# Performance work log

Hardware: AMD Instinct MI355X
Metric: run time of the kernel (lower is better)

## Reference

```python
import jax, jax.numpy as jnp
import numpy as np

APP = 21  # app_num, hard-coded in the original forward (x[..., -21:])


def setup_inputs() -> dict:
    key = jax.random.key(0)
    S, F = 1024, 64            # seq_len, feature_num
    INP = F - 21 + 1           # input_size = 44
    H, E = 1024, 512           # hidden_size, embedding_size
    OUT = 1
    ks = jax.random.split(key, 16)
    s = 0.02
    return {
        "x": jax.random.normal(ks[0], (1, S, F), jnp.float32),
        "W_ie": jax.random.normal(ks[1], (E, INP), jnp.float32) * s,
        "b_ie": jnp.zeros((E,), jnp.float32),
        "W_te": jax.random.normal(ks[2], (E, APP * H), jnp.float32) * s,
        "b_te": jnp.zeros((E,), jnp.float32),
        "W_ih0": jax.random.normal(ks[3], (4 * H, 2 * E), jnp.float32) * s,
        "W_hh0": jax.random.normal(ks[4], (4 * H, H), jnp.float32) * s,
        "b_ih0": jnp.zeros((4 * H,), jnp.float32),
        "b_hh0": jnp.zeros((4 * H,), jnp.float32),
        "W_ih1": jax.random.normal(ks[5], (4 * H, H), jnp.float32) * s,
        "W_hh1": jax.random.normal(ks[6], (4 * H, H), jnp.float32) * s,
        "b_ih1": jnp.zeros((4 * H,), jnp.float32),
        "b_hh1": jnp.zeros((4 * H,), jnp.float32),
        "W_out": jax.random.normal(ks[7], (OUT, APP * H), jnp.float32) * s,
        "b_out": jnp.zeros((OUT,), jnp.float32),
    }


def _lstm_cell(xt, h, c, W_ih, W_hh, b_ih, b_hh):
    # PyTorch gate order: i, f, g, o
    gates = xt @ W_ih.T + b_ih + h @ W_hh.T + b_hh  # [APP, 4H]
    i, f, g, o = jnp.split(gates, 4, axis=-1)
    c_new = jax.nn.sigmoid(f) * c + jax.nn.sigmoid(i) * jnp.tanh(g)
    h_new = jax.nn.sigmoid(o) * jnp.tanh(c_new)
    return h_new, c_new


def reference(x, W_ie, b_ie, W_te, b_te, W_ih0, W_hh0, b_ih0, b_hh0,
              W_ih1, W_hh1, b_ih1, b_hh1, W_out, b_out):
    # eval-mode: dropout is identity (both embedding dropout and LSTM inter-layer dropout)
    S = x.shape[1]
    H = W_hh0.shape[1]
    E = W_ie.shape[0]

    feats = x[0, :, :-APP]                                   # [S, F-21]
    feats = jnp.broadcast_to(feats[:, None, :], (S, APP, feats.shape[-1]))
    app = x[0, :, -APP:][:, :, None]                          # [S, 21, 1]
    input_data = jnp.concatenate([feats, app], axis=-1)       # [S, 21, INP]

    h0 = jnp.zeros((APP, H), x.dtype)
    c0 = jnp.zeros((APP, H), x.dtype)
    h1 = jnp.zeros((APP, H), x.dtype)
    c1 = jnp.zeros((APP, H), x.dtype)

    def step(carry, xt):
        h0, c0, h1, c1 = carry
        # social tensor: last-layer hidden flattened, identical row for all 21 apps
        social = h1.reshape(-1)                               # [21*H]
        te = jax.nn.relu(W_te @ social + b_te)                # [E]
        ie = jax.nn.relu(xt @ W_ie.T + b_ie)                  # [21, E]
        z = jnp.concatenate([ie, jnp.broadcast_to(te, (APP, E))], axis=-1)  # [21, 2E]
        h0n, c0n = _lstm_cell(z, h0, c0, W_ih0, W_hh0, b_ih0, b_hh0)
        h1n, c1n = _lstm_cell(h0n, h1, c1, W_ih1, W_hh1, b_ih1, b_hh1)
        out = W_out @ h1n.reshape(-1) + b_out                 # [output_size]
        return (h0n, c0n, h1n, c1n), out

    (h0, c0, h1, c1), outs = jax.lax.scan(step, (h0, c0, h1, c1), input_data)
    outputs = outs[None, :, :]                                # [1, S, output_size]
    hidden = jnp.stack([h0, h1], axis=0)                      # [num_layer, 21, H]
    cell = jnp.stack([c0, c1], axis=0)
    return outputs, (hidden, cell)
```

## Files before the change

kernel.cpp:

```cpp
#include <hip/hip_runtime.h>
#include <math.h>


#define NBLK 256
#define NTHR 512
#define HTHR 256
#define SEQ  1024
#define HID  1024
#define EMB  512
#define NAG  21
#define NH   21504

#define IE_OFF  0
#define H0_OFF  11010048
#define H1_OFF  (H0_OFF + 2*NH)
#define TE_OFF  (H1_OFF + 2*NH)
#define BAR_OFF (TE_OFF + 512)
#define ZTOT    (4*NH + 512 + 1024)

#define HROW   1152
#define IEROW  576
#define OFF_H    0
#define OFF_IE   24192
#define OFF_TE   36288
#define OFF_PART 36864
#define OFF_B0   39888
#define OFF_B1   39904
#define OFF_RED  39920
#define OFF_ABT  39936
#define LDS_F    39952

#define REP4(M)  M(0) M(1) M(2) M(3)
#define REP8(M)  REP4(M) M(4) M(5) M(6) M(7)
#define REP10(M) REP8(M) M(8) M(9)
#define REP16(M) REP8(M) M(8) M(9) M(10) M(11) M(12) M(13) M(14) M(15)
#define REP40(M) REP16(M) M(16) M(17) M(18) M(19) M(20) M(21) M(22) M(23) \
  M(24) M(25) M(26) M(27) M(28) M(29) M(30) M(31) M(32) M(33) M(34) M(35) \
  M(36) M(37) M(38) M(39)

typedef unsigned u32x4 __attribute__((ext_vector_type(4)));
typedef unsigned u32x2 __attribute__((ext_vector_type(2)));

struct Params {
  const float *x, *W_ie, *b_ie, *W_te, *b_te;
  const float *W_ih0, *W_hh0, *b_ih0, *b_hh0;
  const float *W_ih1, *W_hh1, *b_ih1, *b_hh1;
  const float *W_out, *b_out;
  float *out, *ws;
};

__device__ __forceinline__ float sigf(float v) { return 1.0f / (1.0f + expf(-v)); }

__device__ __forceinline__ float ald(const float* p) {
  return __hip_atomic_load(p, __ATOMIC_RELAXED, __HIP_MEMORY_SCOPE_AGENT);
}
__device__ __forceinline__ void ast(float* p, float v) {
  __hip_atomic_store(p, v, __ATOMIC_RELAXED, __HIP_MEMORY_SCOPE_AGENT);
}
__device__ __forceinline__ unsigned f2bf(float f) {
  unsigned u = __float_as_uint(f);
  return (u + 0x7fffu + ((u >> 16) & 1u)) >> 16;
}

__device__ __forceinline__ float block_sum(float v, float* red) {
  #pragma unroll
  for (int off = 32; off > 0; off >>= 1) v += __shfl_down(v, off, 64);
  const int w = threadIdx.x >> 6;
  if ((threadIdx.x & 63) == 0) red[w] = v;
  __syncthreads();
  float r = 0.f;
  #pragma unroll
  for (int i = 0; i < NTHR / 64; ++i) r += red[i];
  __syncthreads();
  return r;
}

__device__ __forceinline__ void block_sum2(float& v0, float& v1, float* red) {
  #pragma unroll
  for (int off = 32; off > 0; off >>= 1) {
    v0 += __shfl_down(v0, off, 64);
    v1 += __shfl_down(v1, off, 64);
  }
  const int w = threadIdx.x >> 6;
  if ((threadIdx.x & 63) == 0) { red[2 * w] = v0; red[2 * w + 1] = v1; }
  __syncthreads();
  v0 = ((red[0] + red[2]) + (red[4] + red[6])) + ((red[8] + red[10]) + (red[12] + red[14]));
  v1 = ((red[1] + red[3]) + (red[5] + red[7])) + ((red[9] + red[11]) + (red[13] + red[15]));
  __syncthreads();
}

__device__ __forceinline__ bool grid_barrier(unsigned* bars, unsigned ep, int b,
                                             float* ldsf) {
  __syncthreads();
  if (threadIdx.x == 0) {
    float abortv = 0.f;
    unsigned* grel = bars + 512 + ((unsigned)b >> 4) * 32;
    if (__hip_atomic_load(bars + 300, __ATOMIC_RELAXED, __HIP_MEMORY_SCOPE_AGENT) != 0u) {
      abortv = 1.f;
    } else {
      asm volatile("s_waitcnt vmcnt(0)" ::: "memory");
      unsigned* gc = bars + 16 + ((unsigned)b >> 4) * 16;
      unsigned old = __hip_atomic_fetch_add(gc, 1u, __ATOMIC_RELAXED, __HIP_MEMORY_SCOPE_AGENT);
      if (old == ep * 16u - 1u) {
        unsigned rold = __hip_atomic_fetch_add(bars + 16 + 256, 1u, __ATOMIC_RELAXED, __HIP_MEMORY_SCOPE_AGENT);
        if (rold == ep * 16u - 1u) {
          #pragma unroll
          for (int g = 0; g < 16; ++g)
            __hip_atomic_store(bars + 512 + g * 32, ep, __ATOMIC_RELAXED, __HIP_MEMORY_SCOPE_AGENT);
        }
      }
      unsigned spins = 0u;
      while (__hip_atomic_load(grel, __ATOMIC_RELAXED, __HIP_MEMORY_SCOPE_AGENT) < ep) {
        __builtin_amdgcn_s_sleep(8);
        if (++spins > 1000000u) {
          __hip_atomic_store(bars + 300, 1u, __ATOMIC_RELAXED, __HIP_MEMORY_SCOPE_AGENT);
          abortv = 1.f;
          break;
        }
        if ((spins & 255u) == 0u &&
            __hip_atomic_load(bars + 300, __ATOMIC_RELAXED, __HIP_MEMORY_SCOPE_AGENT) != 0u) {
          abortv = 1.f;
          break;
        }
      }
      asm volatile("" ::: "memory");
    }
    ldsf[OFF_ABT] = abortv;
  }
  __syncthreads();
  return ldsf[OFF_ABT] != 0.f;
}

__global__ void sl_init(float* ws) {
  int tid = blockIdx.x * blockDim.x + threadIdx.x;
  int stride = gridDim.x * blockDim.x;
  for (int i = tid; i < ZTOT; i += stride) ws[H0_OFF + i] = 0.0f;
}

__global__ void sl_ie(const float* __restrict__ x, const float* __restrict__ W_ie,
                      const float* __restrict__ b_ie, float* __restrict__ ws) {
  const int t = blockIdx.x;
  const int tid = threadIdx.x;
  __shared__ float xs[64];
  __shared__ float base[EMB];
  __shared__ float w43[EMB];
  if (tid < 64) xs[tid] = x[t * 64 + tid];
  __syncthreads();
  for (int e = tid; e < EMB; e += HTHR) {
    const float* wr = W_ie + e * 44;
    float acc = b_ie[e];
    #pragma unroll
    for (int k = 0; k < 43; ++k) acc += xs[k] * wr[k];
    base[e] = acc;
    w43[e] = wr[43];
  }
  __syncthreads();
  float* iep = ws + IE_OFF + (size_t)t * (NAG * EMB);
  for (int idx = tid; idx < NAG * EMB; idx += HTHR) {
    int a = idx >> 9, e = idx & 511;
    float v = base[e] + xs[43 + a] * w43[e];
    iep[idx] = v > 0.0f ? v : 0.0f;
  }
}

#define SLDQ(q) { const float4* ap = hs4 + 10 * tid + (q); \
  asm volatile("global_load_dwordx4 %0, %1, off sc0" : "=v"(sv[q]) : "v"(ap)); }
#define SSTQ(q) { int i0 = 40 * tid + 4 * (q); int aa = i0 >> 10; int cc = i0 & 1023; \
  float2 f0v; f0v.x = __uint_as_float(sv[q][0]); f0v.y = __uint_as_float(sv[q][1]); \
  *(float2*)&lds[OFF_H + aa * HROW + 36 * (cc >> 5) + (cc & 31)] = f0v; \
  int i1 = i0 + 2; int a1i = i1 >> 10; int c1i = i1 & 1023; \
  float2 f1v; f1v.x = __uint_as_float(sv[q][2]); f1v.y = __uint_as_float(sv[q][3]); \
  *(float2*)&lds[OFF_H + a1i * HROW + 36 * (c1i >> 5) + (c1i & 31)] = f1v; }
#define STAGE_H(SRC) { \
  const float4* hs4 = (const float4*)(SRC); \
  u32x4 sv[10]; u32x2 sv2; \
  REP10(SLDQ) \
  { const float* ap = (const float*)(SRC) + 20480 + 2 * tid; \
    asm volatile("global_load_dwordx2 %0, %1, off sc0" : "=v"(sv2) : "v"(ap)); } \
  asm volatile("s_waitcnt vmcnt(0)" ::: "memory"); \
  __builtin_amdgcn_sched_barrier(0); \
  REP10(SSTQ) \
  { int i2 = 20480 + 2 * tid; int aa = i2 >> 10; int cc = i2 & 1023; float2 ff; \
    ff.x = __uint_as_float(sv2[0]); ff.y = __uint_as_float(sv2[1]); \
    *(float2*)&lds[OFF_H + aa * HROW + 36 * (cc >> 5) + (cc & 31)] = ff; } }

__global__ void __launch_bounds__(NTHR)
__attribute__((amdgpu_waves_per_eu(2, 2)))
sl_main(Params P) {
  const int b = blockIdx.x;
  const int tid = threadIdx.x;
  float* ws = P.ws;
  float* wste = ws + TE_OFF;
  unsigned* bars = (unsigned*)(ws + BAR_OFF);

  __shared__ float lds[LDS_F];

  const int lane = tid & 63;
  const int wav  = tid >> 6;
  const int n    = tid & 15;
  const int ks   = tid >> 4;
  const int grow = (n >> 2) * HID + 4 * b + (n & 3);

  float w0[64];
  {
    const float* s0 = (ks < 16) ? (P.W_ih0 + (size_t)grow * 1024 + 64 * ks)
                                : (P.W_hh0 + (size_t)grow * 1024 + 64 * (ks - 16));
#define LW0(i) { float4 v = *(const float4*)(s0 + 4*(i)); \
    w0[4*(i)] = v.x; w0[4*(i)+1] = v.y; w0[4*(i)+2] = v.z; w0[4*(i)+3] = v.w; }
    REP16(LW0)
  }
  float w1a[32], w1b[32];
  {
    const float* s1 = P.W_ih1 + (size_t)grow * 1024 + 32 * ks;
    const float* s2 = P.W_hh1 + (size_t)grow * 1024 + 32 * ks;
#define LW1(i) { float4 v = *(const float4*)(s1 + 4*(i)); \
    w1a[4*(i)] = v.x; w1a[4*(i)+1] = v.y; w1a[4*(i)+2] = v.z; w1a[4*(i)+3] = v.w; \
    float4 u = *(const float4*)(s2 + 4*(i)); \
    w1b[4*(i)] = u.x; w1b[4*(i)+1] = u.y; w1b[4*(i)+2] = u.z; w1b[4*(i)+3] = u.w; }
    REP8(LW1)
  }
  unsigned wtepk[42];
  {
    const float* wt0 = P.W_te + (size_t)(2 * b) * NH;
#define LWT(k) { float f0 = wt0[40*tid + (k)]; float f1 = wt0[NH + 40*tid + (k)]; \
    wtepk[k] = f2bf(f0) | (f2bf(f1) << 16); }
    REP40(LWT)
    { int ix = 20480 + 2 * tid;
      wtepk[40] = f2bf(wt0[ix])     | (f2bf(wt0[NH + ix]) << 16);
      wtepk[41] = f2bf(wt0[ix + 1]) | (f2bf(wt0[NH + ix + 1]) << 16); }
  }
  const float bte0 = P.b_te[2 * b], bte1 = P.b_te[2 * b + 1];
  const float bout = P.b_out[0];
  if (tid < 16) {
    int gr = (tid >> 2) * HID + 4 * b + (tid & 3);
    lds[OFF_B0 + tid] = P.b_ih0[gr] + P.b_hh0[gr];
    lds[OFF_B1 + tid] = P.b_ih1[gr] + P.b_hh1[gr];
  }
  __syncthreads();

  int bB_base, bB_astep;
  if (ks < 8)       { bB_base = OFF_IE + 72 * ks;        bB_astep = IEROW; }
  else if (ks < 16) { bB_base = OFF_TE + 72 * (ks - 8);  bB_astep = 0;     }
  else              { bB_base = OFF_H  + 72 * (ks - 16); bB_astep = HROW;  }
  const int bC_base = OFF_H + 36 * ks;

  float c0r = 0.f, c1r = 0.f, h0r = 0.f, h1r = 0.f;
  unsigned ep = 0;

  for (int t = 0; t < SEQ; ++t) {
    const int p = t & 1;

    {
      const float* h1base = ws + H1_OFF + p * NH;
      const float4* h1f4 = (const float4*)h1base;
      u32x4 hv[10]; u32x2 hv2;
#define PALD(q) { const float4* ap = h1f4 + 10 * tid + (q); \
      asm volatile("global_load_dwordx4 %0, %1, off sc0" : "=v"(hv[q]) : "v"(ap)); }
      REP10(PALD)
      { const float* ap = h1base + 20480 + 2 * tid;
        asm volatile("global_load_dwordx2 %0, %1, off sc0" : "=v"(hv2) : "v"(ap)); }
      asm volatile("s_waitcnt vmcnt(0)" ::: "memory");
      __builtin_amdgcn_sched_barrier(0);
      float a0 = 0.f, a1 = 0.f;
#define PHAF(k) { float hvf = __uint_as_float(hv[(k)>>2][(k)&3]); \
      a0 += __uint_as_float(wtepk[k] << 16) * hvf; \
      a1 += __uint_as_float(wtepk[k] & 0xffff0000u) * hvf; }
      REP40(PHAF)
      { float hvf = __uint_as_float(hv2[0]);
        a0 += __uint_as_float(wtepk[40] << 16) * hvf;
        a1 += __uint_as_float(wtepk[40] & 0xffff0000u) * hvf; }
      { float hvf = __uint_as_float(hv2[1]);
        a0 += __uint_as_float(wtepk[41] << 16) * hvf;
        a1 += __uint_as_float(wtepk[41] & 0xffff0000u) * hvf; }
      block_sum2(a0, a1, &lds[OFF_RED]);
      if (tid == 0) {
        float v0 = a0 + bte0, v1 = a1 + bte1;
        v0 = v0 > 0.f ? v0 : 0.f;
        v1 = v1 > 0.f ? v1 : 0.f;
        unsigned long long tv = ((unsigned long long)__float_as_uint(v1) << 32)
                              | (unsigned long long)__float_as_uint(v0);
        __hip_atomic_store((unsigned long long*)(wste + 2 * b), tv,
                           __ATOMIC_RELAXED, __HIP_MEMORY_SCOPE_AGENT);
      }
      if (b == 0) {
        float ao = 0.f;
        if (t > 0) {
          const float4* wo4 = (const float4*)P.W_out;
#define PAO(q) { float4 wv = wo4[10 * tid + (q)]; \
          ao += wv.x * __uint_as_float(hv[q][0]) + wv.y * __uint_as_float(hv[q][1]) \
              + wv.z * __uint_as_float(hv[q][2]) + wv.w * __uint_as_float(hv[q][3]); }
          REP10(PAO)
          const float* woe = P.W_out + 20480 + 2 * tid;
          ao += woe[0] * __uint_as_float(hv2[0]) + woe[1] * __uint_as_float(hv2[1]);
        }
        ao = block_sum(ao, &lds[OFF_RED]);
        if (tid == 0 && t > 0) P.out[t - 1] = ao + bout;
      }
    }
    ++ep; if (grid_barrier(bars, ep, b, lds)) break;

    {
      float tev;
      { const float* ap = wste + tid;
        asm volatile("global_load_dword %0, %1, off sc0" : "=v"(tev) : "v"(ap)); }
      {
        const float4* iep4 =
            (const float4*)(ws + IE_OFF + (size_t)t * (NAG * EMB));
        float4 t40 = iep4[tid];
        float4 t41 = iep4[tid + 512];
        float4 t42 = iep4[tid + 1024];
        float4 t43 = iep4[tid + 1536];
        float4 t44 = iep4[tid + 2048];
        float4 t45 = t40;
        const bool g5 = tid < 128;
        if (g5) t45 = iep4[tid + 2560];
#define IEST(k, reg) { int i4 = tid + 512*(k); int aa = i4 >> 7; int k4 = i4 & 127; \
        *(float4*)&lds[OFF_IE + aa * IEROW + 36 * (k4 >> 3) + 4 * (k4 & 7)] = reg; }
        IEST(0, t40) IEST(1, t41) IEST(2, t42) IEST(3, t43) IEST(4, t44)
        if (g5) IEST(5, t45)
      }
      STAGE_H(ws + H0_OFF + p * NH)
      lds[OFF_TE + 36 * (tid >> 5) + (tid & 31)] = tev;
      __syncthreads();

      int laddr = bB_base;
      for (int a = 0; a < NAG; ++a) {
        float ac0 = 0.f, ac1 = 0.f, ac2 = 0.f, ac3 = 0.f;
#define DOTB(j, ac, woff, zoff) { float4 z = *(const float4*)&lds[laddr + (zoff) + 4*(j)]; \
        ac += w0[(woff)+4*(j)]*z.x;   ac += w0[(woff)+4*(j)+1]*z.y; \
        ac += w0[(woff)+4*(j)+2]*z.z; ac += w0[(woff)+4*(j)+3]*z.w; }
        DOTB(0, ac0, 0, 0)  DOTB(1, ac1, 0, 0)  DOTB(2, ac2, 0, 0)  DOTB(3, ac3, 0, 0)
        DOTB(4, ac0, 0, 0)  DOTB(5, ac1, 0, 0)  DOTB(6, ac2, 0, 0)  DOTB(7, ac3, 0, 0)
        DOTB(0, ac0, 32, 36) DOTB(1, ac1, 32, 36) DOTB(2, ac2, 32, 36) DOTB(3, ac3, 32, 36)
        DOTB(4, ac0, 32, 36) DOTB(5, ac1, 32, 36) DOTB(6, ac2, 32, 36) DOTB(7, ac3, 32, 36)
        float acc = (ac0 + ac1) + (ac2 + ac3);
        acc += __shfl_xor(acc, 16);
        acc += __shfl_xor(acc, 32);
        if (lane < 16) lds[OFF_PART + a * 144 + n * 9 + wav] = acc;
        laddr += bB_astep;
      }
      __syncthreads();
      if (tid < 84) {
        int a = tid >> 2, j = tid & 3;
        const float* pp = &lds[OFF_PART + a * 144];
        float gv0, gv1, gv2, gv3;
#define GATE(base, gg, gv) { float s = lds[(base) + 4*(gg) + j]; \
        s += pp[(4*(gg)+j)*9+0] + pp[(4*(gg)+j)*9+1] + pp[(4*(gg)+j)*9+2] + pp[(4*(gg)+j)*9+3]; \
        s += pp[(4*(gg)+j)*9+4] + pp[(4*(gg)+j)*9+5] + pp[(4*(gg)+j)*9+6] + pp[(4*(gg)+j)*9+7]; \
        gv = s; }
        GATE(OFF_B0, 0, gv0) GATE(OFF_B0, 1, gv1) GATE(OFF_B0, 2, gv2) GATE(OFF_B0, 3, gv3)
        float cn = sigf(gv1) * c0r + sigf(gv0) * tanhf(gv2);
        float hn = sigf(gv3) * tanhf(cn);
        c0r = cn; h0r = hn;
        ast(ws + H0_OFF + (p ^ 1) * NH + a * HID + 4 * b + j, hn);
      }
    }
    ++ep; if (grid_barrier(bars, ep, b, lds)) break;

    {
      STAGE_H(ws + H0_OFF + (p ^ 1) * NH)
      __syncthreads();
      int laddr = bC_base;
      for (int a = 0; a < NAG; ++a) {
        float ac0 = 0.f, ac1 = 0.f;
#define DOTC(j, ac, W) { float4 z = *(const float4*)&lds[laddr + 4*(j)]; \
        ac += W[4*(j)]*z.x; ac += W[4*(j)+1]*z.y; ac += W[4*(j)+2]*z.z; ac += W[4*(j)+3]*z.w; }
        DOTC(0, ac0, w1a) DOTC(1, ac1, w1a) DOTC(2, ac0, w1a) DOTC(3, ac1, w1a)
        DOTC(4, ac0, w1a) DOTC(5, ac1, w1a) DOTC(6, ac0, w1a) DOTC(7, ac1, w1a)
        float acc = ac0 + ac1;
        acc += __shfl_xor(acc, 16);
        acc += __shfl_xor(acc, 32);
        if (lane < 16) lds[OFF_PART + a * 144 + n * 9 + wav] = acc;
        laddr += HROW;
      }
      __syncthreads();
      STAGE_H(ws + H1_OFF + p * NH)
      __syncthreads();
      laddr = bC_base;
      for (int a = 0; a < NAG; ++a) {
        float ac0 = 0.f, ac1 = 0.f;
        DOTC(0, ac0, w1b) DOTC(1, ac1, w1b) DOTC(2, ac0, w1b) DOTC(3, ac1, w1b)
        DOTC(4, ac0, w1b) DOTC(5, ac1, w1b) DOTC(6, ac0, w1b) DOTC(7, ac1, w1b)
        float acc = ac0 + ac1;
        acc += __shfl_xor(acc, 16);
        acc += __shfl_xor(acc, 32);
        if (lane < 16) lds[OFF_PART + a * 144 + n * 9 + wav] += acc;
        laddr += HROW;
      }
      __syncthreads();
      if (tid < 84) {
        int a = tid >> 2, j = tid & 3;
        const float* pp = &lds[OFF_PART + a * 144];
        float gv0, gv1, gv2, gv3;
        GATE(OFF_B1, 0, gv0) GATE(OFF_B1, 1, gv1) GATE(OFF_B1, 2, gv2) GATE(OFF_B1, 3, gv3)
        float cn = sigf(gv1) * c1r + sigf(gv0) * tanhf(gv2);
        float hn = sigf(gv3) * tanhf(cn);
        c1r = cn; h1r = hn;
        ast(ws + H1_OFF + (p ^ 1) * NH + a * HID + 4 * b + j, hn);
      }
    }
    ++ep; if (grid_barrier(bars, ep, b, lds)) break;
  }

  if (b == 0) {
    const float* h1s = ws + H1_OFF;
    float ao = 0.f;
    #pragma unroll
    for (int k = 0; k < 42; ++k)
      ao += P.W_out[512 * k + tid] * ald(h1s + 512 * k + tid);
    ao = block_sum(ao, &lds[OFF_RED]);
    if (tid == 0) P.out[SEQ - 1] = ao + bout;
  }
  if (tid < 84) {
    int a = tid >> 2, j = tid & 3;
    int idx = a * HID + 4 * b + j;
    P.out[SEQ + idx]          = h0r;
    P.out[SEQ + NH + idx]     = h1r;
    P.out[SEQ + 2*NH + idx]   = c0r;
    P.out[SEQ + 3*NH + idx]   = c1r;
  }
}

extern "C" void kernel_launch(void* const* d_in, const int* in_sizes, int n_in,
                              void* d_out, int out_size, void* d_ws, size_t ws_size,
                              hipStream_t stream) {
  (void)in_sizes; (void)n_in; (void)out_size; (void)ws_size;
  Params P;
  P.x     = (const float*)d_in[0];
  P.W_ie  = (const float*)d_in[1];
  P.b_ie  = (const float*)d_in[2];
  P.W_te  = (const float*)d_in[3];
  P.b_te  = (const float*)d_in[4];
  P.W_ih0 = (const float*)d_in[5];
  P.W_hh0 = (const float*)d_in[6];
  P.b_ih0 = (const float*)d_in[7];
  P.b_hh0 = (const float*)d_in[8];
  P.W_ih1 = (const float*)d_in[9];
  P.W_hh1 = (const float*)d_in[10];
  P.b_ih1 = (const float*)d_in[11];
  P.b_hh1 = (const float*)d_in[12];
  P.W_out = (const float*)d_in[13];
  P.b_out = (const float*)d_in[14];
  P.out   = (float*)d_out;
  P.ws    = (float*)d_ws;

  sl_init<<<64, HTHR, 0, stream>>>((float*)d_ws);
  sl_ie<<<SEQ, HTHR, 0, stream>>>(P.x, P.W_ie, P.b_ie, (float*)d_ws);

  void* args[] = { &P };
  hipLaunchCooperativeKernel((const void*)sl_main, dim3(NBLK), dim3(NTHR),
                             args, 0, stream);
}
```

Before: 55.30 ms.

## Exchange LSTM hidden states across blocks as packed bf16 and reuse h1 loads

Hidden states h0/h1 passed between blocks through global memory are now stored as bf16, with four values packed into one 64-bit atomic store via lane shuffles. Each block reads half the bytes per staging step. The h1 values already loaded for the social-tensor projection are reused to fill LDS for the layer-1 recurrent matmul instead of being reloaded. This cuts global traffic and latency on the per-step critical path between grid barriers, but rounds the recurrent hidden state to bf16, which adds numerical error across 1024 steps.

```diff
diff --git a/kernel.cpp b/kernel.cpp
--- a/kernel.cpp
+++ b/kernel.cpp
@@ -13,10 +13,9 @@
 
 #define IE_OFF  0
 #define H0_OFF  11010048
-#define H1_OFF  (H0_OFF + 2*NH)
-#define TE_OFF  (H1_OFF + 2*NH)
+#define TE_OFF  (H0_OFF + 43008)
 #define BAR_OFF (TE_OFF + 512)
-#define ZTOT    (4*NH + 512 + 1024)
+#define ZTOT    (43008 + 512 + 1024)
 
 #define HROW   1152
 #define IEROW  576
@@ -31,15 +30,15 @@
 #define LDS_F    39952
 
 #define REP4(M)  M(0) M(1) M(2) M(3)
+#define REP5(M)  REP4(M) M(4)
 #define REP8(M)  REP4(M) M(4) M(5) M(6) M(7)
-#define REP10(M) REP8(M) M(8) M(9)
 #define REP16(M) REP8(M) M(8) M(9) M(10) M(11) M(12) M(13) M(14) M(15)
-#define REP40(M) REP16(M) M(16) M(17) M(18) M(19) M(20) M(21) M(22) M(23) \
+#define REP20(M) REP16(M) M(16) M(17) M(18) M(19)
+#define REP40(M) REP20(M) M(20) M(21) M(22) M(23) \
   M(24) M(25) M(26) M(27) M(28) M(29) M(30) M(31) M(32) M(33) M(34) M(35) \
   M(36) M(37) M(38) M(39)
 
 typedef unsigned u32x4 __attribute__((ext_vector_type(4)));
-typedef unsigned u32x2 __attribute__((ext_vector_type(2)));
 
 struct Params {
   const float *x, *W_ie, *b_ie, *W_te, *b_te;
@@ -50,13 +49,8 @@
 };
 
 __device__ __forceinline__ float sigf(float v) { return 1.0f / (1.0f + expf(-v)); }
-
-__device__ __forceinline__ float ald(const float* p) {
-  return __hip_atomic_load(p, __ATOMIC_RELAXED, __HIP_MEMORY_SCOPE_AGENT);
-}
-__device__ __forceinline__ void ast(float* p, float v) {
-  __hip_atomic_store(p, v, __ATOMIC_RELAXED, __HIP_MEMORY_SCOPE_AGENT);
-}
+__device__ __forceinline__ float bfl(unsigned u) { return __uint_as_float(u << 16); }
+__device__ __forceinline__ float bfh(unsigned u) { return __uint_as_float(u & 0xffff0000u); }
 __device__ __forceinline__ unsigned f2bf(float f) {
   unsigned u = __float_as_uint(f);
   return (u + 0x7fffu + ((u >> 16) & 1u)) >> 16;
@@ -163,26 +157,23 @@
   }
 }
 
-#define SLDQ(q) { const float4* ap = hs4 + 10 * tid + (q); \
+#define HBLD(q) { const u32x4* ap = (const u32x4*)(srcu + 20 * tid) + (q); \
   asm volatile("global_load_dwordx4 %0, %1, off sc0" : "=v"(sv[q]) : "v"(ap)); }
-#define SSTQ(q) { int i0 = 40 * tid + 4 * (q); int aa = i0 >> 10; int cc = i0 & 1023; \
-  float2 f0v; f0v.x = __uint_as_float(sv[q][0]); f0v.y = __uint_as_float(sv[q][1]); \
-  *(float2*)&lds[OFF_H + aa * HROW + 36 * (cc >> 5) + (cc & 31)] = f0v; \
-  int i1 = i0 + 2; int a1i = i1 >> 10; int c1i = i1 & 1023; \
-  float2 f1v; f1v.x = __uint_as_float(sv[q][2]); f1v.y = __uint_as_float(sv[q][3]); \
-  *(float2*)&lds[OFF_H + a1i * HROW + 36 * (c1i >> 5) + (c1i & 31)] = f1v; }
-#define STAGE_H(SRC) { \
-  const float4* hs4 = (const float4*)(SRC); \
-  u32x4 sv[10]; u32x2 sv2; \
-  REP10(SLDQ) \
-  { const float* ap = (const float*)(SRC) + 20480 + 2 * tid; \
-    asm volatile("global_load_dwordx2 %0, %1, off sc0" : "=v"(sv2) : "v"(ap)); } \
+#define ST2(u, e0) { int aa = (e0) >> 10; int cc = (e0) & 1023; float2 f2v; \
+  f2v.x = bfl(u); f2v.y = bfh(u); \
+  *(float2*)&lds[OFF_H + aa * HROW + 36 * (cc >> 5) + (cc & 31)] = f2v; }
+#define HBST(q) { ST2(sv[q][0], 40*tid + 8*(q)) ST2(sv[q][1], 40*tid + 8*(q)+2) \
+  ST2(sv[q][2], 40*tid + 8*(q)+4) ST2(sv[q][3], 40*tid + 8*(q)+6) }
+#define STAGE_HBF(SRCU) { \
+  const unsigned* srcu = (SRCU); \
+  u32x4 sv[5]; unsigned sv2; \
+  REP5(HBLD) \
+  { const unsigned* ap = srcu + 10240 + tid; \
+    asm volatile("global_load_dword %0, %1, off sc0" : "=v"(sv2) : "v"(ap)); } \
   asm volatile("s_waitcnt vmcnt(0)" ::: "memory"); \
   __builtin_amdgcn_sched_barrier(0); \
-  REP10(SSTQ) \
-  { int i2 = 20480 + 2 * tid; int aa = i2 >> 10; int cc = i2 & 1023; float2 ff; \
-    ff.x = __uint_as_float(sv2[0]); ff.y = __uint_as_float(sv2[1]); \
-    *(float2*)&lds[OFF_H + aa * HROW + 36 * (cc >> 5) + (cc & 31)] = ff; } }
+  REP5(HBST) \
+  ST2(sv2, 20480 + 2 * tid) }
 
 __global__ void __launch_bounds__(NTHR)
 __attribute__((amdgpu_waves_per_eu(2, 2)))
@@ -191,6 +182,7 @@
   const int tid = threadIdx.x;
   float* ws = P.ws;
   float* wste = ws + TE_OFF;
+  unsigned* hbase = (unsigned*)(ws + H0_OFF);
   unsigned* bars = (unsigned*)(ws + BAR_OFF);
 
   __shared__ float lds[LDS_F];
@@ -249,29 +241,27 @@
 
   for (int t = 0; t < SEQ; ++t) {
     const int p = t & 1;
+    u32x4 hv[5]; unsigned hv2;
 
     {
-      const float* h1base = ws + H1_OFF + p * NH;
-      const float4* h1f4 = (const float4*)h1base;
-      u32x4 hv[10]; u32x2 hv2;
-#define PALD(q) { const float4* ap = h1f4 + 10 * tid + (q); \
+      const unsigned* h1u = hbase + 21504 + p * 10752;
+#define PALD(q) { const u32x4* ap = (const u32x4*)(h1u + 20 * tid) + (q); \
       asm volatile("global_load_dwordx4 %0, %1, off sc0" : "=v"(hv[q]) : "v"(ap)); }
-      REP10(PALD)
-      { const float* ap = h1base + 20480 + 2 * tid;
-        asm volatile("global_load_dwordx2 %0, %1, off sc0" : "=v"(hv2) : "v"(ap)); }
+      REP5(PALD)
+      { const unsigned* ap = h1u + 10240 + tid;
+        asm volatile("global_load_dword %0, %1, off sc0" : "=v"(hv2) : "v"(ap)); }
       asm volatile("s_waitcnt vmcnt(0)" ::: "memory");
       __builtin_amdgcn_sched_barrier(0);
       float a0 = 0.f, a1 = 0.f;
-#define PHAF(k) { float hvf = __uint_as_float(hv[(k)>>2][(k)&3]); \
-      a0 += __uint_as_float(wtepk[k] << 16) * hvf; \
-      a1 += __uint_as_float(wtepk[k] & 0xffff0000u) * hvf; }
+#define PHAF(k) { unsigned hu = hv[(k) >> 3][((k) >> 1) & 3]; \
+      float hvf = ((k) & 1) ? bfh(hu) : bfl(hu); \
+      a0 += bfl(wtepk[k]) * hvf; \
+      a1 += bfh(wtepk[k]) * hvf; }
       REP40(PHAF)
-      { float hvf = __uint_as_float(hv2[0]);
-        a0 += __uint_as_float(wtepk[40] << 16) * hvf;
-        a1 += __uint_as_float(wtepk[40] & 0xffff0000u) * hvf; }
-      { float hvf = __uint_as_float(hv2[1]);
-        a0 += __uint_as_float(wtepk[41] << 16) * hvf;
-        a1 += __uint_as_float(wtepk[41] & 0xffff0000u) * hvf; }
+      { float hvf = bfl(hv2);
+        a0 += bfl(wtepk[40]) * hvf; a1 += bfh(wtepk[40]) * hvf; }
+      { float hvf = bfh(hv2);
+        a0 += bfl(wtepk[41]) * hvf; a1 += bfh(wtepk[41]) * hvf; }
       block_sum2(a0, a1, &lds[OFF_RED]);
       if (tid == 0) {
         float v0 = a0 + bte0, v1 = a1 + bte1;
@@ -285,13 +275,12 @@
       if (b == 0) {
         float ao = 0.f;
         if (t > 0) {
-          const float4* wo4 = (const float4*)P.W_out;
-#define PAO(q) { float4 wv = wo4[10 * tid + (q)]; \
-          ao += wv.x * __uint_as_float(hv[q][0]) + wv.y * __uint_as_float(hv[q][1]) \
-              + wv.z * __uint_as_float(hv[q][2]) + wv.w * __uint_as_float(hv[q][3]); }
-          REP10(PAO)
+#define PAO(m) { float2 wv = *(const float2*)(P.W_out + 40 * tid + 2 * (m)); \
+          unsigned hu = hv[(m) >> 2][(m) & 3]; \
+          ao += wv.x * bfl(hu) + wv.y * bfh(hu); }
+          REP20(PAO)
           const float* woe = P.W_out + 20480 + 2 * tid;
-          ao += woe[0] * __uint_as_float(hv2[0]) + woe[1] * __uint_as_float(hv2[1]);
+          ao += woe[0] * bfl(hv2) + woe[1] * bfh(hv2);
         }
         ao = block_sum(ao, &lds[OFF_RED]);
         if (tid == 0 && t > 0) P.out[t - 1] = ao + bout;
@@ -319,7 +308,7 @@
         IEST(0, t40) IEST(1, t41) IEST(2, t42) IEST(3, t43) IEST(4, t44)
         if (g5) IEST(5, t45)
       }
-      STAGE_H(ws + H0_OFF + p * NH)
+      STAGE_HBF(hbase + p * 10752)
       lds[OFF_TE + 36 * (tid >> 5) + (tid & 31)] = tev;
       __syncthreads();
 
@@ -352,13 +341,23 @@
         float cn = sigf(gv1) * c0r + sigf(gv0) * tanhf(gv2);
         float hn = sigf(gv3) * tanhf(cn);
         c0r = cn; h0r = hn;
-        ast(ws + H0_OFF + (p ^ 1) * NH + a * HID + 4 * b + j, hn);
+        unsigned hb16 = f2bf(hn);
+        unsigned nb1 = __shfl_down(hb16, 1, 64);
+        unsigned nb2 = __shfl_down(hb16, 2, 64);
+        unsigned nb3 = __shfl_down(hb16, 3, 64);
+        if (j == 0) {
+          unsigned long long pk = (unsigned long long)hb16
+            | ((unsigned long long)nb1 << 16) | ((unsigned long long)nb2 << 32)
+            | ((unsigned long long)nb3 << 48);
+          __hip_atomic_store((unsigned long long*)(hbase + (p ^ 1) * 10752) + (a * 256 + b),
+                             pk, __ATOMIC_RELAXED, __HIP_MEMORY_SCOPE_AGENT);
+        }
       }
     }
     ++ep; if (grid_barrier(bars, ep, b, lds)) break;
 
     {
-      STAGE_H(ws + H0_OFF + (p ^ 1) * NH)
+      STAGE_HBF(hbase + (p ^ 1) * 10752)
       __syncthreads();
       int laddr = bC_base;
       for (int a = 0; a < NAG; ++a) {
@@ -374,7 +373,12 @@
         laddr += HROW;
       }
       __syncthreads();
-      STAGE_H(ws + H1_OFF + p * NH)
+      {
+#define RSTB(q) { ST2(hv[q][0], 40*tid + 8*(q)) ST2(hv[q][1], 40*tid + 8*(q)+2) \
+        ST2(hv[q][2], 40*tid + 8*(q)+4) ST2(hv[q][3], 40*tid + 8*(q)+6) }
+        REP5(RSTB)
+        ST2(hv2, 20480 + 2 * tid)
+      }
       __syncthreads();
       laddr = bC_base;
       for (int a = 0; a < NAG; ++a) {
@@ -396,18 +400,39 @@
         float cn = sigf(gv1) * c1r + sigf(gv0) * tanhf(gv2);
         float hn = sigf(gv3) * tanhf(cn);
         c1r = cn; h1r = hn;
-        ast(ws + H1_OFF + (p ^ 1) * NH + a * HID + 4 * b + j, hn);
+        unsigned hb16 = f2bf(hn);
+        unsigned nb1 = __shfl_down(hb16, 1, 64);
+        unsigned nb2 = __shfl_down(hb16, 2, 64);
+        unsigned nb3 = __shfl_down(hb16, 3, 64);
+        if (j == 0) {
+          unsigned long long pk = (unsigned long long)hb16
+            | ((unsigned long long)nb1 << 16) | ((unsigned long long)nb2 << 32)
+            | ((unsigned long long)nb3 << 48);
+          __hip_atomic_store((unsigned long long*)(hbase + 21504 + (p ^ 1) * 10752) + (a * 256 + b),
+                             pk, __ATOMIC_RELAXED, __HIP_MEMORY_SCOPE_AGENT);
+        }
       }
     }
     ++ep; if (grid_barrier(bars, ep, b, lds)) break;
   }
 
   if (b == 0) {
-    const float* h1s = ws + H1_OFF;
+    const unsigned* h1u = hbase + 21504;
+    u32x4 ev[5]; unsigned ev2;
+#define ELD(q) { const u32x4* ap = (const u32x4*)(h1u + 20 * tid) + (q); \
+    asm volatile("global_load_dwordx4 %0, %1, off sc0" : "=v"(ev[q]) : "v"(ap)); }
+    REP5(ELD)
+    { const unsigned* ap = h1u + 10240 + tid;
+      asm volatile("global_load_dword %0, %1, off sc0" : "=v"(ev2) : "v"(ap)); }
+    asm volatile("s_waitcnt vmcnt(0)" ::: "memory");
+    __builtin_amdgcn_sched_barrier(0);
     float ao = 0.f;
-    #pragma unroll
-    for (int k = 0; k < 42; ++k)
-      ao += P.W_out[512 * k + tid] * ald(h1s + 512 * k + tid);
+#define EAO(m) { float2 wv = *(const float2*)(P.W_out + 40 * tid + 2 * (m)); \
+    unsigned hu = ev[(m) >> 2][(m) & 3]; \
+    ao += wv.x * bfl(hu) + wv.y * bfh(hu); }
+    REP20(EAO)
+    { const float* woe = P.W_out + 20480 + 2 * tid;
+      ao += woe[0] * bfl(ev2) + woe[1] * bfh(ev2); }
     ao = block_sum(ao, &lds[OFF_RED]);
     if (tid == 0) P.out[SEQ - 1] = ao + bout;
   }
```

Result: faster. 52.51 ms (median of 2 runs) (-5.0%).
